# Kernel optimization log

Measured on AMD Instinct MI355X. Metric: run time of the kernel, lower is better.

The kernel has to match this reference:

```python
import jax, jax.numpy as jnp
import numpy as np

B, S, H, KV, D, HID = 1, 2048, 32, 8, 128, 4096
SCALE = D ** -0.5
EPS = 1e-5
QMAX = 127.0  # 8-bit symmetric fake quant


def fake_quant(x):
    # per-tensor symmetric int8 fake quantization with straight-through estimator
    s = jnp.maximum(jnp.max(jnp.abs(x)), 1e-5) / QMAX
    q = jnp.clip(jnp.round(x / s), -QMAX - 1.0, QMAX) * s
    return x + jax.lax.stop_gradient(q - x)


def rms_norm(x, w):
    xf = x.astype(jnp.float32)
    var = jnp.mean(xf * xf, axis=-1, keepdims=True)
    return (xf * jax.lax.rsqrt(var + EPS)).astype(x.dtype) * w


def rotate_half(x):
    h = x.shape[-1] // 2
    return jnp.concatenate([-x[..., h:], x[..., :h]], axis=-1)


def qlinear(x, W):
    # QuantLinear: fake-quant activation and weight, then matmul (no bias)
    return fake_quant(x) @ fake_quant(W).T


def setup_inputs() -> dict:
    key = jax.random.key(0)
    ks = jax.random.split(key, 5)
    hidden_states = jax.random.normal(ks[0], (B, S, HID), jnp.float32)
    # RoPE tables
    inv_freq = 1.0 / (10000.0 ** (np.arange(0, D, 2, dtype=np.float32) / D))
    freqs = np.outer(np.arange(S, dtype=np.float32), inv_freq)  # [S, D/2]
    emb = np.concatenate([freqs, freqs], axis=-1)  # [S, D]
    cos = jnp.asarray(np.cos(emb))[None]  # [1,S,D]
    sin = jnp.asarray(np.sin(emb))[None]
    # causal additive mask [1,1,S,S]
    mask = jnp.where(np.tril(np.ones((S, S), dtype=bool)), 0.0, -1e9).astype(jnp.float32)[None, None]
    Wq = jax.random.normal(ks[1], (H * D, HID), jnp.float32) * 0.02
    Wk = jax.random.normal(ks[2], (KV * D, HID), jnp.float32) * 0.02
    Wv = jax.random.normal(ks[3], (KV * D, HID), jnp.float32) * 0.02
    Wo = jax.random.normal(ks[4], (HID, H * D), jnp.float32) * 0.02
    q_norm_w = jnp.ones((D,), jnp.float32)
    k_norm_w = jnp.ones((D,), jnp.float32)
    return dict(hidden_states=hidden_states, cos=cos, sin=sin, attention_mask=mask,
                Wq=Wq, Wk=Wk, Wv=Wv, Wo=Wo, q_norm_w=q_norm_w, k_norm_w=k_norm_w)


def reference(hidden_states, cos, sin, attention_mask, Wq, Wk, Wv, Wo, q_norm_w, k_norm_w):
    b, s, _ = hidden_states.shape
    q = qlinear(hidden_states, Wq).reshape(b, s, H, D).transpose(0, 2, 1, 3)   # [B,H,S,D]
    k = qlinear(hidden_states, Wk).reshape(b, s, KV, D).transpose(0, 2, 1, 3)  # [B,KV,S,D]
    v = qlinear(hidden_states, Wv).reshape(b, s, KV, D).transpose(0, 2, 1, 3)
    q = rms_norm(q, q_norm_w)
    k = rms_norm(k, k_norm_w)
    c = cos[:, None]  # unsqueeze head dim -> [1,1,S,D]
    sn = sin[:, None]
    q = q * c + rotate_half(q) * sn
    k = k * c + rotate_half(k) * sn
    n_rep = H // KV
    k = jnp.repeat(k, n_rep, axis=1)  # [B,H,S,D]
    v = jnp.repeat(v, n_rep, axis=1)
    # fake-quant around QK^T
    q = fake_quant(q)
    k = fake_quant(k)
    scores = jnp.einsum('bhqd,bhkd->bhqk', q, k) * SCALE + attention_mask
    p = jax.nn.softmax(scores.astype(jnp.float32), axis=-1).astype(q.dtype)
    # fake-quant around PV
    p = fake_quant(p)
    v = fake_quant(v)
    out = jnp.einsum('bhqk,bhkd->bhqd', p, v)
    out = out.transpose(0, 2, 1, 3).reshape(b, s, H * D)
    return qlinear(out, Wo)
```

## Files before the change

### kernel.cpp

```cpp
#include <hip/hip_runtime.h>
#include <hip/hip_bf16.h>
#include <math.h>
#include <stdint.h>

#define S_LEN 2048
#define NH    32
#define NKV   8
#define HD    128
#define HIDD  4096

typedef unsigned short u16;
typedef __attribute__((ext_vector_type(4))) int i32x4;

#define GLD16(g, l) __builtin_amdgcn_global_load_lds( \
    (const __attribute__((address_space(1))) void*)(g), \
    (__attribute__((address_space(3))) void*)(l), 16, 0, 0)


__device__ __forceinline__ float slot_scale(const unsigned* slot) {
    return fmaxf(__uint_as_float(*slot), 1e-5f) / 127.0f;
}

__device__ __forceinline__ float exp2_fast(float x) {
    float r; asm("v_exp_f32 %0, %1" : "=v"(r) : "v"(x)); return r;
}

__device__ __forceinline__ int qint(float x, float s) {
    float q = rintf(x / s);
    q = fminf(fmaxf(q, -128.0f), 127.0f);
    return (int)q;
}

__device__ __forceinline__ void block_amax_atomic(float m, unsigned* slot) {
    __shared__ float wmax[8];
    const int lane = threadIdx.x & 63;
    const int wid  = threadIdx.x >> 6;
    const int nw   = blockDim.x >> 6;
    #pragma unroll
    for (int o = 32; o; o >>= 1) m = fmaxf(m, __shfl_xor(m, o));
    if (lane == 0) wmax[wid] = m;
    __syncthreads();
    if (threadIdx.x == 0) {
        float bm = wmax[0];
        for (int i = 1; i < nw; ++i) bm = fmaxf(bm, wmax[i]);
        atomicMax(slot, __float_as_uint(bm));
    }
}

struct Amax5Args { const float* p[5]; size_t n4[5]; };
__global__ __launch_bounds__(256) void absmax5_kernel(Amax5Args a, unsigned* slots) {
    const int t = blockIdx.y;
    const float4* x4 = (const float4*)a.p[t];
    const size_t n4 = a.n4[t];
    size_t i = (size_t)blockIdx.x * blockDim.x + threadIdx.x;
    size_t stride = (size_t)gridDim.x * blockDim.x;
    float m = 0.0f;
    for (; i < n4; i += stride) {
        float4 v = x4[i];
        m = fmaxf(m, fmaxf(fmaxf(fabsf(v.x), fabsf(v.y)), fmaxf(fabsf(v.z), fabsf(v.w))));
    }
    block_amax_atomic(m, slots + t);
}

struct Quant5Args { const float* p[5]; char* o[5]; size_t n4[5]; };
__global__ __launch_bounds__(256) void quant5_kernel(Quant5Args a, const unsigned* slots) {
    const int t = blockIdx.y;
    float s = slot_scale(slots + t);
    const float4* x4 = (const float4*)a.p[t];
    unsigned* o4 = (unsigned*)a.o[t];
    const size_t n4 = a.n4[t];
    size_t i = (size_t)blockIdx.x * blockDim.x + threadIdx.x;
    size_t stride = (size_t)gridDim.x * blockDim.x;
    for (; i < n4; i += stride) {
        float4 v = x4[i];
        unsigned o = (unsigned)(qint(v.x, s) & 255)
                   | ((unsigned)(qint(v.y, s) & 255) << 8)
                   | ((unsigned)(qint(v.z, s) & 255) << 16)
                   | ((unsigned)(qint(v.w, s) & 255) << 24);
        o4[i] = o;
    }
}

__global__ __launch_bounds__(256) void quant_kernel(const float* __restrict__ x,
                                                    size_t n4, const unsigned* slot,
                                                    char* __restrict__ out) {
    float s = slot_scale(slot);
    size_t i = (size_t)blockIdx.x * blockDim.x + threadIdx.x;
    size_t stride = (size_t)gridDim.x * blockDim.x;
    const float4* x4 = (const float4*)x;
    unsigned* o4 = (unsigned*)out;
    for (; i < n4; i += stride) {
        float4 v = x4[i];
        unsigned o = (unsigned)(qint(v.x, s) & 255)
                   | ((unsigned)(qint(v.y, s) & 255) << 8)
                   | ((unsigned)(qint(v.z, s) & 255) << 16)
                   | ((unsigned)(qint(v.w, s) & 255) << 24);
        o4[i] = o;
    }
}

__device__ __forceinline__ void gemm_body(const char* __restrict__ A,
                                          const char* __restrict__ B,
                                          float* __restrict__ C,
                                          int m0, int n0, int N, int K,
                                          float scale, unsigned* out_amax,
                                          char* Asm, char* Bsm) {
    const int tid  = threadIdx.x;
    const int lane = tid & 63;
    const int wave = tid >> 6;
    const int wr = (wave >> 1) * 64;
    const int wc = (wave & 1) * 64;
    const int l15 = lane & 15;
    const int l4  = lane >> 4;
    const int cx  = (l4 ^ (l15 & 3)) * 16;
    const int r0  = tid >> 2;
    const int sc  = ((tid & 3) ^ ((tid >> 2) & 3)) * 16;

    i32x4 acc[4][4];
    #pragma unroll
    for (int i = 0; i < 4; ++i)
        #pragma unroll
        for (int j = 0; j < 4; ++j) acc[i][j] = (i32x4){0, 0, 0, 0};

    auto STAGE = [&](int buf, int k0) {
        GLD16(&A[(size_t)(m0 + r0) * K + k0 + sc],      &Asm[buf * 8192 + wave * 1024]);
        GLD16(&A[(size_t)(m0 + 64 + r0) * K + k0 + sc], &Asm[buf * 8192 + 4096 + wave * 1024]);
        GLD16(&B[(size_t)(n0 + r0) * K + k0 + sc],      &Bsm[buf * 8192 + wave * 1024]);
        GLD16(&B[(size_t)(n0 + 64 + r0) * K + k0 + sc], &Bsm[buf * 8192 + 4096 + wave * 1024]);
    };

    STAGE(0, 0);
    __syncthreads();
    int cur = 0;
    const int NT = K >> 6;
    for (int t = 0; t < NT; ++t) {
        if (t + 1 < NT) STAGE(cur ^ 1, (t + 1) << 6);
        i32x4 af[4], bfr[4];
        #pragma unroll
        for (int i = 0; i < 4; ++i)
            af[i] = *(const i32x4*)&Asm[cur * 8192 + (wr + i * 16 + l15) * 64 + cx];
        #pragma unroll
        for (int j = 0; j < 4; ++j)
            bfr[j] = *(const i32x4*)&Bsm[cur * 8192 + (wc + j * 16 + l15) * 64 + cx];
        #pragma unroll
        for (int i = 0; i < 4; ++i)
            #pragma unroll
            for (int j = 0; j < 4; ++j)
                acc[i][j] = __builtin_amdgcn_mfma_i32_16x16x64_i8(af[i], bfr[j], acc[i][j], 0, 0, 0);
        __syncthreads();
        cur ^= 1;
    }

    float lm = 0.0f;
    #pragma unroll
    for (int i = 0; i < 4; ++i)
        #pragma unroll
        for (int j = 0; j < 4; ++j)
            #pragma unroll
            for (int r = 0; r < 4; ++r) {
                int row = m0 + wr + i * 16 + l4 * 4 + r;
                int col = n0 + wc + j * 16 + l15;
                float v = (float)acc[i][j][r] * scale;
                C[(size_t)row * N + col] = v;
                lm = fmaxf(lm, fabsf(v));
            }
    if (out_amax) block_amax_atomic(lm, out_amax);
}

__global__ __launch_bounds__(256) void gemm_qkv_kernel(const char* __restrict__ Aq,
                                                       const char* __restrict__ Wqq,
                                                       const char* __restrict__ Wkq,
                                                       const char* __restrict__ Wvq,
                                                       float* __restrict__ qf,
                                                       float* __restrict__ kf,
                                                       float* __restrict__ vf,
                                                       const unsigned* __restrict__ slots,
                                                       unsigned* v_amax) {
    __shared__ __align__(16) char Asm[2 * 8192];
    __shared__ __align__(16) char Bsm[2 * 8192];
    int bid = blockIdx.x;
    int swz = (bid & 7) * 96 + (bid >> 3);
    int x = swz & 15, y = swz >> 4;
    const char* B; float* C; int N, nb; const unsigned* sB; unsigned* am = nullptr;
    if (y < 32)      { B = Wqq; C = qf; N = NH * HD;  nb = y;      sB = slots + 1; }
    else if (y < 40) { B = Wkq; C = kf; N = NKV * HD; nb = y - 32; sB = slots + 2; }
    else             { B = Wvq; C = vf; N = NKV * HD; nb = y - 40; sB = slots + 3; am = v_amax; }
    float scale = slot_scale(slots + 0) * slot_scale(sB);
    gemm_body(Aq, B, C, x * 128, nb * 128, N, HIDD, scale, am, Asm, Bsm);
}

__global__ __launch_bounds__(256) void gemm_o_kernel(const char* __restrict__ A,
                                                     const char* __restrict__ Woq,
                                                     float* __restrict__ C,
                                                     const unsigned* __restrict__ slots) {
    __shared__ __align__(16) char Asm[2 * 8192];
    __shared__ __align__(16) char Bsm[2 * 8192];
    int bid = blockIdx.x;
    int swz = (bid & 7) * 64 + (bid >> 3);
    int x = swz & 15, y = swz >> 4;
    float scale = slot_scale(slots + 8) * slot_scale(slots + 4);
    gemm_body(A, Woq, C, x * 128, y * 128, NH * HD, HIDD, scale, nullptr, Asm, Bsm);
}

__global__ __launch_bounds__(256) void rmsrope2_kernel(float* __restrict__ qx,
                                                       float* __restrict__ kx,
                                                       const float* __restrict__ cosb,
                                                       const float* __restrict__ sinb,
                                                       const float* __restrict__ qw,
                                                       const float* __restrict__ kw,
                                                       unsigned* slots) {
    const int which = blockIdx.y;
    float* x = which ? kx : qx;
    const float* w = which ? kw : qw;
    const int s_shift = which ? 3 : 5;
    const int nrows = which ? (S_LEN * NKV) : (S_LEN * NH);
    unsigned* slot = slots + (which ? 6 : 5);

    const int lane = threadIdx.x & 63;
    const int wid  = threadIdx.x >> 6;
    const float wa = w[lane];
    const float wb = w[lane + 64];
    float lm = 0.0f;
    for (int row = blockIdx.x * 4 + wid; row < nrows; row += gridDim.x * 4) {
        int s = row >> s_shift;
        float* xr = x + (size_t)row * 128;
        float a = xr[lane], b = xr[lane + 64];
        float ss = a * a + b * b;
        #pragma unroll
        for (int o = 32; o; o >>= 1) ss += __shfl_xor(ss, o);
        float inv = 1.0f / sqrtf(ss * (1.0f / 128.0f) + 1e-5f);
        float ya = (a * inv) * wa;
        float yb = (b * inv) * wb;
        const float* cr = cosb + (size_t)s * 128;
        const float* sr = sinb + (size_t)s * 128;
        float o0 = ya * cr[lane]      - yb * sr[lane];
        float o1 = yb * cr[lane + 64] + ya * sr[lane + 64];
        xr[lane] = o0;
        xr[lane + 64] = o1;
        lm = fmaxf(lm, fmaxf(fabsf(o0), fabsf(o1)));
    }
    block_amax_atomic(lm, slot);
}

__global__ __launch_bounds__(256) void quant_qk2_kernel(const float* __restrict__ qx,
                                                        const float* __restrict__ kx,
                                                        const unsigned* slots,
                                                        char* __restrict__ qq,
                                                        char* __restrict__ kq) {
    int tid = blockIdx.x * 256 + threadIdx.x;
    const int qtot = S_LEN * NH * HD;
    if (tid < qtot) {
        float s = slot_scale(slots + 5);
        int d  = tid & 127;
        int h  = (tid >> 7) & 31;
        int sp = tid >> 12;
        qq[((size_t)h * S_LEN + sp) * 128 + d] = (char)qint(qx[tid], s);
    } else {
        tid -= qtot;
        float s = slot_scale(slots + 6);
        int d  = tid & 127;
        int h  = (tid >> 7) & 7;
        int sp = tid >> 10;
        kq[((size_t)h * S_LEN + sp) * 128 + d] = (char)qint(kx[tid], s);
    }
}

__global__ __launch_bounds__(256) void quant_v_kernel(const float* __restrict__ x,
                                                      const unsigned* slot,
                                                      char* __restrict__ out) {
    __shared__ unsigned char t8[64][36];
    const float s = slot_scale(slot);
    const int t   = threadIdx.x;
    const int sp0 = blockIdx.x * 64;
    const int d0  = blockIdx.y * 32;
    const int kvh = blockIdx.z;
    const int dl = t & 31;
    const int sb = t >> 5;
    #pragma unroll
    for (int j = 0; j < 8; ++j) {
        int spl = sb + j * 8;
        float v = x[((size_t)(sp0 + spl) * NKV + kvh) * 128 + d0 + dl];
        t8[spl][dl] = (unsigned char)qint(v, s);
    }
    __syncthreads();
    const int dd = t >> 3;
    const int ch = t & 7;
    unsigned lo = 0, hi = 0;
    #pragma unroll
    for (int j = 0; j < 4; ++j) lo |= (unsigned)t8[ch * 8 + j][dd] << (8 * j);
    #pragma unroll
    for (int j = 0; j < 4; ++j) hi |= (unsigned)t8[ch * 8 + 4 + j][dd] << (8 * j);
    *(uint2*)&out[((size_t)kvh * 128 + d0 + dd) * S_LEN + sp0 + ch * 8] = make_uint2(lo, hi);
}

__global__ __launch_bounds__(256) void attn_kernel(const char* __restrict__ Qq,
                                                   const char* __restrict__ Kq,
                                                   const char* __restrict__ Vt,
                                                   const unsigned* sq_slot,
                                                   const unsigned* sk_slot,
                                                   const unsigned* sv_slot,
                                                   float* __restrict__ O,
                                                   unsigned* amax_slot) {
    __shared__ __align__(16) char Klds[64 * 144];
    __shared__ __align__(16) char Vlds[128 * 80];
    __shared__ __align__(16) char plds[4][16 * 80];

    const int tid  = threadIdx.x;
    const int lane = tid & 63;
    const int wave = tid >> 6;
    const int h  = blockIdx.y;
    const int kv = h >> 2;
    const int l15 = lane & 15;
    const int l4  = lane >> 4;
    const size_t kvS = (size_t)kv * S_LEN;

    const float sq = slot_scale(sq_slot);
    const float sk = slot_scale(sk_slot);
    const float sv = slot_scale(sv_slot);
    const float qs2 = sq * sk * 0.08838834764831845f * 1.4426950408889634f;
    const float osc = (1.0f / 127.0f) * sv;
    const float NEG = -1e30f;

    float lm = 0.0f;

    #pragma unroll 1
    for (int tpass = 0; tpass < 2; ++tpass) {
        const int qt  = tpass ? (31 - (int)blockIdx.x) : (int)blockIdx.x;
        const int qr0 = qt * 64 + wave * 16;
        const int nchunk = qt + 1;

        i32x4 qf2[2];
        {
            const char* qp = Qq + ((size_t)h * S_LEN + qr0 + l15) * 128 + l4 * 16;
            qf2[0] = *(const i32x4*)(qp);
            qf2[1] = *(const i32x4*)(qp + 64);
        }

        float m_l = NEG, l_l = 0.0f;

        auto qk_block = [&](int hb) -> i32x4 {
            i32x4 sacc = {0, 0, 0, 0};
            #pragma unroll
            for (int c = 0; c < 2; ++c) {
                i32x4 kfa = *(const i32x4*)&Klds[(hb * 16 + l15) * 144 + c * 64 + l4 * 16];
                sacc = __builtin_amdgcn_mfma_i32_16x16x64_i8(kfa, qf2[c], sacc, 0, 0, 0);
            }
            return sacc;
        };
        auto p1_interior = [&](int hb) {
            i32x4 sacc = qk_block(hb);
            float x0 = (float)sacc[0] * qs2, x1 = (float)sacc[1] * qs2;
            float x2 = (float)sacc[2] * qs2, x3 = (float)sacc[3] * qs2;
            float bm = fmaxf(fmaxf(x0, x1), fmaxf(x2, x3));
            float mn = fmaxf(m_l, bm);
            float ps = exp2_fast(x0 - mn) + exp2_fast(x1 - mn)
                     + exp2_fast(x2 - mn) + exp2_fast(x3 - mn);
            l_l = l_l * exp2_fast(m_l - mn) + ps;
            m_l = mn;
        };
        auto p1_diag = [&](int hb) {
            i32x4 sacc = qk_block(hb);
            float x[4];
            #pragma unroll
            for (int r = 0; r < 4; ++r) {
                float v = (float)sacc[r] * qs2;
                x[r] = ((l4 * 4 + r) > l15) ? NEG : v;
            }
            float bm = fmaxf(fmaxf(x[0], x[1]), fmaxf(x[2], x[3]));
            float mn = fmaxf(m_l, bm);
            float ps = exp2_fast(x[0] - mn) + exp2_fast(x[1] - mn)
                     + exp2_fast(x[2] - mn) + exp2_fast(x[3] - mn);
            l_l = l_l * exp2_fast(m_l - mn) + ps;
            m_l = mn;
        };

        i32x4 kreg[2];
        #pragma unroll
        for (int c = 0; c < 2; ++c) {
            int idx = c * 256 + tid;
            kreg[c] = *(const i32x4*)&Kq[(kvS + (idx >> 3)) * 128 + (idx & 7) * 16];
        }
        #pragma unroll 1
        for (int kc = 0; kc < nchunk; ++kc) {
            __syncthreads();
            #pragma unroll
            for (int c = 0; c < 2; ++c) {
                int idx = c * 256 + tid;
                *(i32x4*)&Klds[(idx >> 3) * 144 + (idx & 7) * 16] = kreg[c];
            }
            __syncthreads();
            if (kc + 1 < nchunk) {
                #pragma unroll
                for (int c = 0; c < 2; ++c) {
                    int idx = c * 256 + tid;
                    kreg[c] = *(const i32x4*)&Kq[(kvS + (kc + 1) * 64 + (idx >> 3)) * 128 + (idx & 7) * 16];
                }
            }
            if (kc < qt) {
                p1_interior(0); p1_interior(1); p1_interior(2); p1_interior(3);
            } else {
                #pragma unroll
                for (int hb = 0; hb < 4; ++hb) {
                    if (hb < wave) p1_interior(hb);
                    else if (hb == wave) p1_diag(hb);
                }
            }
        }
        float m2 = fmaxf(m_l, __shfl_xor(m_l, 16));
        float mfin = fmaxf(m2, __shfl_xor(m2, 32));
        float t = l_l * exp2_fast(m_l - mfin);
        t += __shfl_xor(t, 16);
        t += __shfl_xor(t, 32);
        float rl = 127.0f / t;

        i32x4 oacc[8];
        #pragma unroll
        for (int dt = 0; dt < 8; ++dt) oacc[dt] = (i32x4){0, 0, 0, 0};

        auto p2_interior = [&](int hb) -> unsigned {
            i32x4 sacc = qk_block(hb);
            unsigned pack = 0;
            #pragma unroll
            for (int r = 0; r < 4; ++r) {
                float x = (float)sacc[r] * qs2;
                float pq = rintf(exp2_fast(x - mfin) * rl);
                pack |= ((unsigned)(int)pq) << (8 * r);
            }
            return pack;
        };
        auto p2_diag = [&](int hb) -> unsigned {
            i32x4 sacc = qk_block(hb);
            unsigned pack = 0;
            #pragma unroll
            for (int r = 0; r < 4; ++r) {
                float x = (float)sacc[r] * qs2;
                float p = exp2_fast(x - mfin) * rl;
                float pq = ((l4 * 4 + r) > l15) ? 0.0f : rintf(p);
                pack |= ((unsigned)(int)pq) << (8 * r);
            }
            return pack;
        };

        i32x4 vreg[2];
        #pragma unroll
        for (int c = 0; c < 2; ++c) {
            int idx = c * 256 + tid;
            kreg[c] = *(const i32x4*)&Kq[(kvS + (idx >> 3)) * 128 + (idx & 7) * 16];
            vreg[c] = *(const i32x4*)&Vt[((size_t)kv * 128 + (idx >> 2)) * S_LEN + (idx & 3) * 16];
        }
        #pragma unroll 1
        for (int kc = 0; kc < nchunk; ++kc) {
            __syncthreads();
            #pragma unroll
            for (int c = 0; c < 2; ++c) {
                int idx = c * 256 + tid;
                *(i32x4*)&Klds[(idx >> 3) * 144 + (idx & 7) * 16] = kreg[c];
                *(i32x4*)&Vlds[(idx >> 2) * 80 + (idx & 3) * 16] = vreg[c];
            }
            __syncthreads();
            if (kc + 1 < nchunk) {
                #pragma unroll
                for (int c = 0; c < 2; ++c) {
                    int idx = c * 256 + tid;
                    kreg[c] = *(const i32x4*)&Kq[(kvS + (kc + 1) * 64 + (idx >> 3)) * 128 + (idx & 7) * 16];
                    vreg[c] = *(const i32x4*)&Vt[((size_t)kv * 128 + (idx >> 2)) * S_LEN + (kc + 1) * 64 + (idx & 3) * 16];
                }
            }
            if (kc < qt) {
                #pragma unroll
                for (int hb = 0; hb < 4; ++hb)
                    *(unsigned*)&plds[wave][l15 * 80 + hb * 16 + l4 * 4] = p2_interior(hb);
            } else {
                #pragma unroll
                for (int hb = 0; hb < 4; ++hb) {
                    unsigned pack = 0;
                    if (hb < wave) pack = p2_interior(hb);
                    else if (hb == wave) pack = p2_diag(hb);
                    *(unsigned*)&plds[wave][l15 * 80 + hb * 16 + l4 * 4] = pack;
                }
            }
            i32x4 pf = *(const i32x4*)&plds[wave][l15 * 80 + l4 * 16];
            #pragma unroll
            for (int dt = 0; dt < 8; ++dt) {
                i32x4 vfb = *(const i32x4*)&Vlds[(dt * 16 + l15) * 80 + l4 * 16];
                oacc[dt] = __builtin_amdgcn_mfma_i32_16x16x64_i8(pf, vfb, oacc[dt], 0, 0, 0);
            }
        }

        #pragma unroll
        for (int dt = 0; dt < 8; ++dt)
            #pragma unroll
            for (int r = 0; r < 4; ++r) {
                int qrow = qr0 + l4 * 4 + r;
                float v = (float)oacc[dt][r] * osc;
                O[(size_t)qrow * (NH * 128) + h * 128 + dt * 16 + l15] = v;
                lm = fmaxf(lm, fabsf(v));
            }
    }
    block_amax_atomic(lm, amax_slot);
}

extern "C" void kernel_launch(void* const* d_in, const int* in_sizes, int n_in,
                              void* d_out, int out_size, void* d_ws, size_t ws_size,
                              hipStream_t stream) {
    const float* hs   = (const float*)d_in[0];
    const float* cosb = (const float*)d_in[1];
    const float* sinb = (const float*)d_in[2];
    const float* Wq   = (const float*)d_in[4];
    const float* Wk   = (const float*)d_in[5];
    const float* Wv   = (const float*)d_in[6];
    const float* Wo   = (const float*)d_in[7];
    const float* qnw  = (const float*)d_in[8];
    const float* knw  = (const float*)d_in[9];
    float* out = (float*)d_out;

    char* ws = (char*)d_ws;
    unsigned* slots = (unsigned*)ws;
    size_t off = 256;
    auto take = [&](size_t bytes) { size_t o = off; off += (bytes + 255) & ~(size_t)255; return o; };
    char*  hsq  = (char*)(ws + take((size_t)S_LEN * HIDD));
    char*  Wqq  = (char*)(ws + take((size_t)NH * HD * HIDD));
    char*  Wkq  = (char*)(ws + take((size_t)NKV * HD * HIDD));
    char*  Wvq  = (char*)(ws + take((size_t)NKV * HD * HIDD));
    char*  Woq  = (char*)(ws + take((size_t)HIDD * NH * HD));
    float* qf   = (float*)(ws + take((size_t)S_LEN * NH * HD * 4));
    float* kf   = (float*)(ws + take((size_t)S_LEN * NKV * HD * 4));
    float* vf   = (float*)(ws + take((size_t)S_LEN * NKV * HD * 4));
    char*  qq   = (char*)(ws + take((size_t)NH * S_LEN * HD));
    char*  kq   = (char*)(ws + take((size_t)NKV * S_LEN * HD));
    char*  vtq  = (char*)(ws + take((size_t)NKV * HD * S_LEN));
    float* attnf = qf;
    char*  attnq = hsq;

    hipMemsetAsync(ws, 0, 64, stream);

    const size_t n_hs = (size_t)S_LEN * HIDD;
    const size_t n_wq = (size_t)NH * HD * HIDD;
    const size_t n_wk = (size_t)NKV * HD * HIDD;

    Amax5Args aa;
    aa.p[0] = hs; aa.p[1] = Wq; aa.p[2] = Wk; aa.p[3] = Wv; aa.p[4] = Wo;
    aa.n4[0] = n_hs / 4; aa.n4[1] = n_wq / 4; aa.n4[2] = n_wk / 4;
    aa.n4[3] = n_wk / 4; aa.n4[4] = n_wq / 4;
    absmax5_kernel<<<dim3(512, 5), 256, 0, stream>>>(aa, slots);

    Quant5Args qa;
    qa.p[0] = hs; qa.p[1] = Wq; qa.p[2] = Wk; qa.p[3] = Wv; qa.p[4] = Wo;
    qa.o[0] = hsq; qa.o[1] = Wqq; qa.o[2] = Wkq; qa.o[3] = Wvq; qa.o[4] = Woq;
    qa.n4[0] = n_hs / 4; qa.n4[1] = n_wq / 4; qa.n4[2] = n_wk / 4;
    qa.n4[3] = n_wk / 4; qa.n4[4] = n_wq / 4;
    quant5_kernel<<<dim3(1024, 5), 256, 0, stream>>>(qa, slots);

    gemm_qkv_kernel<<<768, 256, 0, stream>>>(hsq, Wqq, Wkq, Wvq, qf, kf, vf,
                                             slots, slots + 7);

    rmsrope2_kernel<<<dim3(1024, 2), 256, 0, stream>>>(qf, kf, cosb, sinb, qnw, knw, slots);

    quant_qk2_kernel<<<40960, 256, 0, stream>>>(qf, kf, slots, qq, kq);
    quant_v_kernel<<<dim3(32, 4, 8), 256, 0, stream>>>(vf, slots + 7, vtq);

    attn_kernel<<<dim3(16, NH), 256, 0, stream>>>(qq, kq, vtq,
                                                  slots + 5, slots + 6, slots + 7,
                                                  attnf, slots + 8);

    quant_kernel<<<2048, 256, 0, stream>>>(attnf, n_hs / 4, slots + 8, attnq);
    gemm_o_kernel<<<512, 256, 0, stream>>>(attnq, Woq, out, slots);
    (void)in_sizes; (void)n_in; (void)out_size; (void)ws_size;
}
```

Baseline: 361.2 us.

## Triple-buffer GEMM loads, vectorize QK quant, merge attention passes into 512-thread blocks

The int8 GEMM moves from a double-buffered LDS pipeline to a triple-buffered one. It waits with explicit vmcnt and uses a single barrier per k-step, so global loads run two tiles ahead of the MFMAs. The Q/K quant kernel now handles four elements per thread with float4 loads and uchar4 stores, and launches a quarter of the blocks. The attention kernel processes both causal query tiles at once using 8 waves, with the K/V staging shared between them, instead of two sequential passes. It also folds the 127/l normalization into the exp2 exponent through a log2. These changes cost more LDS per GEMM block and more registers per attention block, and the log2 fold can shift p-quantization rounding slightly.

```diff
diff --git a/kernel.cpp b/kernel.cpp
--- a/kernel.cpp
+++ b/kernel.cpp
@@ -23,6 +23,9 @@
 
 __device__ __forceinline__ float exp2_fast(float x) {
     float r; asm("v_exp_f32 %0, %1" : "=v"(r) : "v"(x)); return r;
+}
+__device__ __forceinline__ float log2_fast(float x) {
+    float r; asm("v_log_f32 %0, %1" : "=v"(r) : "v"(x)); return r;
 }
 
 __device__ __forceinline__ int qint(float x, float s) {
@@ -129,12 +132,23 @@
         GLD16(&B[(size_t)(n0 + 64 + r0) * K + k0 + sc], &Bsm[buf * 8192 + 4096 + wave * 1024]);
     };
 
+    const int NT = K >> 6;
     STAGE(0, 0);
-    __syncthreads();
+    STAGE(1, 64);
     int cur = 0;
-    const int NT = K >> 6;
     for (int t = 0; t < NT; ++t) {
-        if (t + 1 < NT) STAGE(cur ^ 1, (t + 1) << 6);
+        if (t + 1 < NT) {
+            asm volatile("s_waitcnt vmcnt(4)" ::: "memory");
+        } else {
+            asm volatile("s_waitcnt vmcnt(0)" ::: "memory");
+        }
+        __builtin_amdgcn_sched_barrier(0);
+        __builtin_amdgcn_s_barrier();
+        __builtin_amdgcn_sched_barrier(0);
+        if (t + 2 < NT) {
+            int nb = cur + 2; if (nb >= 3) nb -= 3;
+            STAGE(nb, (t + 2) << 6);
+        }
         i32x4 af[4], bfr[4];
         #pragma unroll
         for (int i = 0; i < 4; ++i)
@@ -147,8 +161,7 @@
             #pragma unroll
             for (int j = 0; j < 4; ++j)
                 acc[i][j] = __builtin_amdgcn_mfma_i32_16x16x64_i8(af[i], bfr[j], acc[i][j], 0, 0, 0);
-        __syncthreads();
-        cur ^= 1;
+        cur += 1; if (cur == 3) cur = 0;
     }
 
     float lm = 0.0f;
@@ -164,6 +177,7 @@
                 C[(size_t)row * N + col] = v;
                 lm = fmaxf(lm, fabsf(v));
             }
+    __syncthreads();
     if (out_amax) block_amax_atomic(lm, out_amax);
 }
 
@@ -176,8 +190,8 @@
                                                        float* __restrict__ vf,
                                                        const unsigned* __restrict__ slots,
                                                        unsigned* v_amax) {
-    __shared__ __align__(16) char Asm[2 * 8192];
-    __shared__ __align__(16) char Bsm[2 * 8192];
+    __shared__ __align__(16) char Asm[3 * 8192];
+    __shared__ __align__(16) char Bsm[3 * 8192];
     int bid = blockIdx.x;
     int swz = (bid & 7) * 96 + (bid >> 3);
     int x = swz & 15, y = swz >> 4;
@@ -193,8 +207,8 @@
                                                      const char* __restrict__ Woq,
                                                      float* __restrict__ C,
                                                      const unsigned* __restrict__ slots) {
-    __shared__ __align__(16) char Asm[2 * 8192];
-    __shared__ __align__(16) char Bsm[2 * 8192];
+    __shared__ __align__(16) char Asm[3 * 8192];
+    __shared__ __align__(16) char Bsm[3 * 8192];
     int bid = blockIdx.x;
     int swz = (bid & 7) * 64 + (bid >> 3);
     int x = swz & 15, y = swz >> 4;
@@ -248,20 +262,30 @@
                                                         char* __restrict__ qq,
                                                         char* __restrict__ kq) {
     int tid = blockIdx.x * 256 + threadIdx.x;
-    const int qtot = S_LEN * NH * HD;
-    if (tid < qtot) {
+    const int qtot4 = S_LEN * NH * HD / 4;
+    if (tid < qtot4) {
         float s = slot_scale(slots + 5);
-        int d  = tid & 127;
-        int h  = (tid >> 7) & 31;
-        int sp = tid >> 12;
-        qq[((size_t)h * S_LEN + sp) * 128 + d] = (char)qint(qx[tid], s);
+        int e = tid * 4;
+        int d  = e & 127;
+        int h  = (e >> 7) & 31;
+        int sp = e >> 12;
+        float4 v = *(const float4*)&qx[e];
+        uchar4 o;
+        o.x = (unsigned char)qint(v.x, s); o.y = (unsigned char)qint(v.y, s);
+        o.z = (unsigned char)qint(v.z, s); o.w = (unsigned char)qint(v.w, s);
+        *(uchar4*)&qq[((size_t)h * S_LEN + sp) * 128 + d] = o;
     } else {
-        tid -= qtot;
+        tid -= qtot4;
         float s = slot_scale(slots + 6);
-        int d  = tid & 127;
-        int h  = (tid >> 7) & 7;
-        int sp = tid >> 10;
-        kq[((size_t)h * S_LEN + sp) * 128 + d] = (char)qint(kx[tid], s);
+        int e = tid * 4;
+        int d  = e & 127;
+        int h  = (e >> 7) & 7;
+        int sp = e >> 10;
+        float4 v = *(const float4*)&kx[e];
+        uchar4 o;
+        o.x = (unsigned char)qint(v.x, s); o.y = (unsigned char)qint(v.y, s);
+        o.z = (unsigned char)qint(v.z, s); o.w = (unsigned char)qint(v.w, s);
+        *(uchar4*)&kq[((size_t)h * S_LEN + sp) * 128 + d] = o;
     }
 }
 
@@ -293,7 +317,7 @@
     *(uint2*)&out[((size_t)kvh * 128 + d0 + dd) * S_LEN + sp0 + ch * 8] = make_uint2(lo, hi);
 }
 
-__global__ __launch_bounds__(256) void attn_kernel(const char* __restrict__ Qq,
+__global__ __launch_bounds__(512) void attn_kernel(const char* __restrict__ Qq,
                                                    const char* __restrict__ Kq,
                                                    const char* __restrict__ Vt,
                                                    const unsigned* sq_slot,
@@ -303,16 +327,22 @@
                                                    unsigned* amax_slot) {
     __shared__ __align__(16) char Klds[64 * 144];
     __shared__ __align__(16) char Vlds[128 * 80];
-    __shared__ __align__(16) char plds[4][16 * 80];
+    __shared__ __align__(16) char plds[8][16 * 80];
 
     const int tid  = threadIdx.x;
     const int lane = tid & 63;
     const int wave = tid >> 6;
+    const int mw   = wave & 3;
     const int h  = blockIdx.y;
     const int kv = h >> 2;
     const int l15 = lane & 15;
     const int l4  = lane >> 4;
     const size_t kvS = (size_t)kv * S_LEN;
+
+    const int qtS = blockIdx.x;
+    const int qtB = 31 - qtS;
+    const int my_qt = (wave < 4) ? qtB : qtS;
+    const int qr0 = my_qt * 64 + mw * 16;
 
     const float sq = slot_scale(sq_slot);
     const float sk = slot_scale(sk_slot);
@@ -321,182 +351,157 @@
     const float osc = (1.0f / 127.0f) * sv;
     const float NEG = -1e30f;
 
-    float lm = 0.0f;
-
+    const int krow = tid >> 3, kcol = (tid & 7) * 16;
+    const int vrow = tid >> 2, vcol = (tid & 3) * 16;
+
+    i32x4 qf2[2];
+    {
+        const char* qp = Qq + ((size_t)h * S_LEN + qr0 + l15) * 128 + l4 * 16;
+        qf2[0] = *(const i32x4*)(qp);
+        qf2[1] = *(const i32x4*)(qp + 64);
+    }
+
+    auto qk_block = [&](int hb) -> i32x4 {
+        i32x4 sacc = {0, 0, 0, 0};
+        #pragma unroll
+        for (int c = 0; c < 2; ++c) {
+            i32x4 kfa = *(const i32x4*)&Klds[(hb * 16 + l15) * 144 + c * 64 + l4 * 16];
+            sacc = __builtin_amdgcn_mfma_i32_16x16x64_i8(kfa, qf2[c], sacc, 0, 0, 0);
+        }
+        return sacc;
+    };
+
+    float m_l = NEG, l_l = 0.0f;
+
+    auto p1_interior = [&](int hb) {
+        i32x4 sacc = qk_block(hb);
+        float x0 = (float)sacc[0] * qs2, x1 = (float)sacc[1] * qs2;
+        float x2 = (float)sacc[2] * qs2, x3 = (float)sacc[3] * qs2;
+        float bm = fmaxf(fmaxf(x0, x1), fmaxf(x2, x3));
+        float mn = fmaxf(m_l, bm);
+        float ps = exp2_fast(x0 - mn) + exp2_fast(x1 - mn)
+                 + exp2_fast(x2 - mn) + exp2_fast(x3 - mn);
+        l_l = l_l * exp2_fast(m_l - mn) + ps;
+        m_l = mn;
+    };
+    auto p1_diag = [&](int hb) {
+        i32x4 sacc = qk_block(hb);
+        float x[4];
+        #pragma unroll
+        for (int r = 0; r < 4; ++r) {
+            float v = (float)sacc[r] * qs2;
+            x[r] = ((l4 * 4 + r) > l15) ? NEG : v;
+        }
+        float bm = fmaxf(fmaxf(x[0], x[1]), fmaxf(x[2], x[3]));
+        float mn = fmaxf(m_l, bm);
+        float ps = exp2_fast(x[0] - mn) + exp2_fast(x[1] - mn)
+                 + exp2_fast(x[2] - mn) + exp2_fast(x[3] - mn);
+        l_l = l_l * exp2_fast(m_l - mn) + ps;
+        m_l = mn;
+    };
+
+    i32x4 kreg = *(const i32x4*)&Kq[(kvS + krow) * 128 + kcol];
     #pragma unroll 1
-    for (int tpass = 0; tpass < 2; ++tpass) {
-        const int qt  = tpass ? (31 - (int)blockIdx.x) : (int)blockIdx.x;
-        const int qr0 = qt * 64 + wave * 16;
-        const int nchunk = qt + 1;
-
-        i32x4 qf2[2];
-        {
-            const char* qp = Qq + ((size_t)h * S_LEN + qr0 + l15) * 128 + l4 * 16;
-            qf2[0] = *(const i32x4*)(qp);
-            qf2[1] = *(const i32x4*)(qp + 64);
-        }
-
-        float m_l = NEG, l_l = 0.0f;
-
-        auto qk_block = [&](int hb) -> i32x4 {
-            i32x4 sacc = {0, 0, 0, 0};
+    for (int kc = 0; kc <= qtB; ++kc) {
+        __syncthreads();
+        *(i32x4*)&Klds[krow * 144 + kcol] = kreg;
+        __syncthreads();
+        if (kc < qtB)
+            kreg = *(const i32x4*)&Kq[(kvS + (kc + 1) * 64 + krow) * 128 + kcol];
+        if (kc < my_qt) {
+            p1_interior(0); p1_interior(1); p1_interior(2); p1_interior(3);
+        } else if (kc == my_qt) {
             #pragma unroll
-            for (int c = 0; c < 2; ++c) {
-                i32x4 kfa = *(const i32x4*)&Klds[(hb * 16 + l15) * 144 + c * 64 + l4 * 16];
-                sacc = __builtin_amdgcn_mfma_i32_16x16x64_i8(kfa, qf2[c], sacc, 0, 0, 0);
+            for (int hb = 0; hb < 4; ++hb) {
+                if (hb < mw) p1_interior(hb);
+                else if (hb == mw) p1_diag(hb);
             }
-            return sacc;
-        };
-        auto p1_interior = [&](int hb) {
-            i32x4 sacc = qk_block(hb);
-            float x0 = (float)sacc[0] * qs2, x1 = (float)sacc[1] * qs2;
-            float x2 = (float)sacc[2] * qs2, x3 = (float)sacc[3] * qs2;
-            float bm = fmaxf(fmaxf(x0, x1), fmaxf(x2, x3));
-            float mn = fmaxf(m_l, bm);
-            float ps = exp2_fast(x0 - mn) + exp2_fast(x1 - mn)
-                     + exp2_fast(x2 - mn) + exp2_fast(x3 - mn);
-            l_l = l_l * exp2_fast(m_l - mn) + ps;
-            m_l = mn;
-        };
-        auto p1_diag = [&](int hb) {
-            i32x4 sacc = qk_block(hb);
-            float x[4];
-            #pragma unroll
-            for (int r = 0; r < 4; ++r) {
-                float v = (float)sacc[r] * qs2;
-                x[r] = ((l4 * 4 + r) > l15) ? NEG : v;
-            }
-            float bm = fmaxf(fmaxf(x[0], x[1]), fmaxf(x[2], x[3]));
-            float mn = fmaxf(m_l, bm);
-            float ps = exp2_fast(x[0] - mn) + exp2_fast(x[1] - mn)
-                     + exp2_fast(x[2] - mn) + exp2_fast(x[3] - mn);
-            l_l = l_l * exp2_fast(m_l - mn) + ps;
-            m_l = mn;
-        };
-
-        i32x4 kreg[2];
-        #pragma unroll
-        for (int c = 0; c < 2; ++c) {
-            int idx = c * 256 + tid;
-            kreg[c] = *(const i32x4*)&Kq[(kvS + (idx >> 3)) * 128 + (idx & 7) * 16];
-        }
-        #pragma unroll 1
-        for (int kc = 0; kc < nchunk; ++kc) {
-            __syncthreads();
-            #pragma unroll
-            for (int c = 0; c < 2; ++c) {
-                int idx = c * 256 + tid;
-                *(i32x4*)&Klds[(idx >> 3) * 144 + (idx & 7) * 16] = kreg[c];
-            }
-            __syncthreads();
-            if (kc + 1 < nchunk) {
-                #pragma unroll
-                for (int c = 0; c < 2; ++c) {
-                    int idx = c * 256 + tid;
-                    kreg[c] = *(const i32x4*)&Kq[(kvS + (kc + 1) * 64 + (idx >> 3)) * 128 + (idx & 7) * 16];
-                }
-            }
-            if (kc < qt) {
-                p1_interior(0); p1_interior(1); p1_interior(2); p1_interior(3);
-            } else {
-                #pragma unroll
-                for (int hb = 0; hb < 4; ++hb) {
-                    if (hb < wave) p1_interior(hb);
-                    else if (hb == wave) p1_diag(hb);
-                }
-            }
-        }
+        }
+    }
+    float cmy;
+    {
         float m2 = fmaxf(m_l, __shfl_xor(m_l, 16));
         float mfin = fmaxf(m2, __shfl_xor(m2, 32));
         float t = l_l * exp2_fast(m_l - mfin);
         t += __shfl_xor(t, 16);
         t += __shfl_xor(t, 32);
-        float rl = 127.0f / t;
-
-        i32x4 oacc[8];
-        #pragma unroll
-        for (int dt = 0; dt < 8; ++dt) oacc[dt] = (i32x4){0, 0, 0, 0};
-
-        auto p2_interior = [&](int hb) -> unsigned {
-            i32x4 sacc = qk_block(hb);
-            unsigned pack = 0;
+        cmy = mfin - log2_fast(127.0f / t);
+    }
+
+    i32x4 oacc[8];
+    #pragma unroll
+    for (int dt = 0; dt < 8; ++dt) oacc[dt] = (i32x4){0, 0, 0, 0};
+
+    auto p2_interior = [&](int hb) -> unsigned {
+        i32x4 sacc = qk_block(hb);
+        unsigned pack = 0;
+        #pragma unroll
+        for (int r = 0; r < 4; ++r) {
+            float pq = rintf(exp2_fast(fmaf((float)sacc[r], qs2, -cmy)));
+            pack |= ((unsigned)(int)pq) << (8 * r);
+        }
+        return pack;
+    };
+    auto p2_diag = [&](int hb) -> unsigned {
+        i32x4 sacc = qk_block(hb);
+        unsigned pack = 0;
+        #pragma unroll
+        for (int r = 0; r < 4; ++r) {
+            float p = exp2_fast(fmaf((float)sacc[r], qs2, -cmy));
+            float pq = ((l4 * 4 + r) > l15) ? 0.0f : rintf(p);
+            pack |= ((unsigned)(int)pq) << (8 * r);
+        }
+        return pack;
+    };
+    auto pv8 = [&]() {
+        i32x4 pf = *(const i32x4*)&plds[wave][l15 * 80 + l4 * 16];
+        __builtin_amdgcn_s_setprio(1);
+        #pragma unroll
+        for (int dt = 0; dt < 8; ++dt) {
+            i32x4 vfb = *(const i32x4*)&Vlds[(dt * 16 + l15) * 80 + l4 * 16];
+            oacc[dt] = __builtin_amdgcn_mfma_i32_16x16x64_i8(pf, vfb, oacc[dt], 0, 0, 0);
+        }
+        __builtin_amdgcn_s_setprio(0);
+    };
+
+    kreg = *(const i32x4*)&Kq[(kvS + krow) * 128 + kcol];
+    i32x4 vreg = *(const i32x4*)&Vt[((size_t)kv * 128 + vrow) * S_LEN + vcol];
+    #pragma unroll 1
+    for (int kc = 0; kc <= qtB; ++kc) {
+        __syncthreads();
+        *(i32x4*)&Klds[krow * 144 + kcol] = kreg;
+        *(i32x4*)&Vlds[vrow * 80 + vcol] = vreg;
+        __syncthreads();
+        if (kc < qtB) {
+            kreg = *(const i32x4*)&Kq[(kvS + (kc + 1) * 64 + krow) * 128 + kcol];
+            vreg = *(const i32x4*)&Vt[((size_t)kv * 128 + vrow) * S_LEN + (kc + 1) * 64 + vcol];
+        }
+        if (kc < my_qt) {
             #pragma unroll
-            for (int r = 0; r < 4; ++r) {
-                float x = (float)sacc[r] * qs2;
-                float pq = rintf(exp2_fast(x - mfin) * rl);
-                pack |= ((unsigned)(int)pq) << (8 * r);
+            for (int hb = 0; hb < 4; ++hb)
+                *(unsigned*)&plds[wave][l15 * 80 + hb * 16 + l4 * 4] = p2_interior(hb);
+            pv8();
+        } else if (kc == my_qt) {
+            #pragma unroll
+            for (int hb = 0; hb < 4; ++hb) {
+                unsigned pack = 0;
+                if (hb < mw) pack = p2_interior(hb);
+                else if (hb == mw) pack = p2_diag(hb);
+                *(unsigned*)&plds[wave][l15 * 80 + hb * 16 + l4 * 4] = pack;
             }
-            return pack;
-        };
-        auto p2_diag = [&](int hb) -> unsigned {
-            i32x4 sacc = qk_block(hb);
-            unsigned pack = 0;
-            #pragma unroll
-            for (int r = 0; r < 4; ++r) {
-                float x = (float)sacc[r] * qs2;
-                float p = exp2_fast(x - mfin) * rl;
-                float pq = ((l4 * 4 + r) > l15) ? 0.0f : rintf(p);
-                pack |= ((unsigned)(int)pq) << (8 * r);
-            }
-            return pack;
-        };
-
-        i32x4 vreg[2];
-        #pragma unroll
-        for (int c = 0; c < 2; ++c) {
-            int idx = c * 256 + tid;
-            kreg[c] = *(const i32x4*)&Kq[(kvS + (idx >> 3)) * 128 + (idx & 7) * 16];
-            vreg[c] = *(const i32x4*)&Vt[((size_t)kv * 128 + (idx >> 2)) * S_LEN + (idx & 3) * 16];
-        }
-        #pragma unroll 1
-        for (int kc = 0; kc < nchunk; ++kc) {
-            __syncthreads();
-            #pragma unroll
-            for (int c = 0; c < 2; ++c) {
-                int idx = c * 256 + tid;
-                *(i32x4*)&Klds[(idx >> 3) * 144 + (idx & 7) * 16] = kreg[c];
-                *(i32x4*)&Vlds[(idx >> 2) * 80 + (idx & 3) * 16] = vreg[c];
-            }
-            __syncthreads();
-            if (kc + 1 < nchunk) {
-                #pragma unroll
-                for (int c = 0; c < 2; ++c) {
-                    int idx = c * 256 + tid;
-                    kreg[c] = *(const i32x4*)&Kq[(kvS + (kc + 1) * 64 + (idx >> 3)) * 128 + (idx & 7) * 16];
-                    vreg[c] = *(const i32x4*)&Vt[((size_t)kv * 128 + (idx >> 2)) * S_LEN + (kc + 1) * 64 + (idx & 3) * 16];
-                }
-            }
-            if (kc < qt) {
-                #pragma unroll
-                for (int hb = 0; hb < 4; ++hb)
-                    *(unsigned*)&plds[wave][l15 * 80 + hb * 16 + l4 * 4] = p2_interior(hb);
-            } else {
-                #pragma unroll
-                for (int hb = 0; hb < 4; ++hb) {
-                    unsigned pack = 0;
-                    if (hb < wave) pack = p2_interior(hb);
-                    else if (hb == wave) pack = p2_diag(hb);
-                    *(unsigned*)&plds[wave][l15 * 80 + hb * 16 + l4 * 4] = pack;
-                }
-            }
-            i32x4 pf = *(const i32x4*)&plds[wave][l15 * 80 + l4 * 16];
-            #pragma unroll
-            for (int dt = 0; dt < 8; ++dt) {
-                i32x4 vfb = *(const i32x4*)&Vlds[(dt * 16 + l15) * 80 + l4 * 16];
-                oacc[dt] = __builtin_amdgcn_mfma_i32_16x16x64_i8(pf, vfb, oacc[dt], 0, 0, 0);
-            }
-        }
-
-        #pragma unroll
-        for (int dt = 0; dt < 8; ++dt)
-            #pragma unroll
-            for (int r = 0; r < 4; ++r) {
-                int qrow = qr0 + l4 * 4 + r;
-                float v = (float)oacc[dt][r] * osc;
-                O[(size_t)qrow * (NH * 128) + h * 128 + dt * 16 + l15] = v;
-                lm = fmaxf(lm, fabsf(v));
-            }
-    }
+            pv8();
+        }
+    }
+
+    float lm = 0.0f;
+    #pragma unroll
+    for (int dt = 0; dt < 8; ++dt)
+        #pragma unroll
+        for (int r = 0; r < 4; ++r) {
+            float v = (float)oacc[dt][r] * osc;
+            O[(size_t)(qr0 + l4 * 4 + r) * (NH * 128) + h * 128 + dt * 16 + l15] = v;
+            lm = fmaxf(lm, fabsf(v));
+        }
     block_amax_atomic(lm, amax_slot);
 }
 
@@ -556,10 +561,10 @@
 
     rmsrope2_kernel<<<dim3(1024, 2), 256, 0, stream>>>(qf, kf, cosb, sinb, qnw, knw, slots);
 
-    quant_qk2_kernel<<<40960, 256, 0, stream>>>(qf, kf, slots, qq, kq);
+    quant_qk2_kernel<<<10240, 256, 0, stream>>>(qf, kf, slots, qq, kq);
     quant_v_kernel<<<dim3(32, 4, 8), 256, 0, stream>>>(vf, slots + 7, vtq);
 
-    attn_kernel<<<dim3(16, NH), 256, 0, stream>>>(qq, kq, vtq,
+    attn_kernel<<<dim3(16, NH), 512, 0, stream>>>(qq, kq, vtq,
                                                   slots + 5, slots + 6, slots + 7,
                                                   attnf, slots + 8);
 
```

New measurement: 343.3 us. -5.0%, faster.
